# Performance work log

Measured on AMD Instinct MI355X. Metric: run time of the kernel, lower is better.

Reference implementation:

```python
import jax, jax.numpy as jnp
import numpy as np


def _mlp(x, W1, b1, W2, b2, W3, b3):
    # flatten -> fc(784,512) -> relu -> fc(512,128) -> relu -> fc(128,C)
    h = x.reshape(x.shape[0], -1)
    h = jax.nn.relu(h @ W1.T + b1)
    h = jax.nn.relu(h @ W2.T + b2)
    return h @ W3.T + b3


def setup_inputs() -> dict:
    key = jax.random.key(0)
    ks = jax.random.split(key, 6)
    B, Bu, C, D = 65536, 4096, 10, 28 * 28
    return {
        "x": jax.random.uniform(ks[0], (B, 28, 28), jnp.float32),
        "y": jax.random.randint(ks[1], (B,), 0, C),
        "x_unlab": jax.random.uniform(ks[2], (Bu, 28, 28), jnp.float32),
        "W1": jax.random.normal(ks[3], (512, D), jnp.float32) * 0.03,
        "b1": jnp.zeros((512,), jnp.float32),
        "W2": jax.random.normal(ks[4], (128, 512), jnp.float32) * 0.05,
        "b2": jnp.zeros((128,), jnp.float32),
        "W3": jax.random.normal(ks[5], (C, 128), jnp.float32) * 0.08,
        "b3": jnp.zeros((C,), jnp.float32),
    }


def reference(x, y, x_unlab, W1, b1, W2, b2, W3, b3):
    n_classes = W3.shape[0]
    # ---- labeled branch: BCEWithLogitsLoss(mean) vs one-hot targets ----
    logits = _mlp(x, W1, b1, W2, b2, W3, b3)  # [B, C]
    t = jax.nn.one_hot(y, n_classes, dtype=logits.dtype)
    bce = jnp.mean(jnp.maximum(logits, 0.0) - logits * t
                   + jnp.log1p(jnp.exp(-jnp.abs(logits))))
    # ---- unlabeled branch: semantic loss ----
    # sem_loss(probs): s[c] = sum_i p_i[c] * prod_{j != i} (1 - p_j[c]);
    # return mean over classes of -log(s). Done in log domain with a single
    # O(Bu) leave-one-out sum instead of the original O(Bu^2) double loop.
    o_u = _mlp(x_unlab, W1, b1, W2, b2, W3, b3)       # [Bu, C]
    logp = jax.nn.log_sigmoid(o_u)                     # log p
    log1mp = jax.nn.log_sigmoid(-o_u)                  # log (1 - p)
    loo = jnp.sum(log1mp, axis=0, keepdims=True) - log1mp  # leave-one-out log-prod
    log_s = jax.scipy.special.logsumexp(logp + loo, axis=0)  # [C]
    sl = jnp.mean(-log_s)
    # compute_loss returns (bce, sl); stacked here as a length-2 vector
    return jnp.stack([bce, sl])
```

## Files before the change

### kernel.cpp

```cpp
#include <hip/hip_runtime.h>
#include <hip/hip_bf16.h>
#include <stdint.h>

typedef unsigned short ushort_t;
typedef __bf16 bf16x8 __attribute__((ext_vector_type(8)));
typedef float f32x4 __attribute__((ext_vector_type(4)));

__device__ __forceinline__ ushort_t f2bf(float f) {
    union { float f; unsigned u; } v; v.f = f;
    unsigned u = v.u;
    unsigned r = u + 0x7fffu + ((u >> 16) & 1u);
    return (ushort_t)(r >> 16);
}
__device__ __forceinline__ float bf2f(ushort_t h) {
    union { unsigned u; float f; } v; v.u = ((unsigned)h) << 16;
    return v.f;
}
__device__ __forceinline__ unsigned packbf(float a, float b) {
    return ((unsigned)f2bf(b) << 16) | f2bf(a);
}

#define GLDS16(gsrc, ldst)                                                    \
    __builtin_amdgcn_global_load_lds(                                         \
        (const __attribute__((address_space(1))) void*)(gsrc),                \
        (__attribute__((address_space(3))) void*)(ldst), 16, 0, 0)

__global__ __launch_bounds__(256) void prep_kernel(
    const float* __restrict__ W1, const float* __restrict__ W2,
    ushort_t* __restrict__ W1p, ushort_t* __restrict__ W2b,
    float* __restrict__ stats)
{
    int idx = blockIdx.x * 256 + threadIdx.x;
    if (idx < 512 * 800) {
        int n = idx / 800, k = idx - n * 800;
        W1p[idx] = (k < 784) ? f2bf(W1[n * 784 + k]) : (ushort_t)0;
    }
    if (idx < 128 * 512) W2b[idx] = f2bf(W2[idx]);
    if (idx == 0) stats[0] = 0.0f;
}

#define AS_STRIDE 36
#define H_STRIDE  136

__global__ __launch_bounds__(256) void fused_kernel(
    const float* __restrict__ x, const float* __restrict__ xu,
    const ushort_t* __restrict__ W1p, const ushort_t* __restrict__ W2b,
    const float* __restrict__ b1, const float* __restrict__ b2,
    const int* __restrict__ y, const float* __restrict__ W3,
    const float* __restrict__ b3,
    float* __restrict__ stats, float* __restrict__ logits_u)
{
    __shared__ ushort_t smem[2 * 64 * AS_STRIDE + 2 * 128 * 32];
    __shared__ float W3s[1280];
    __shared__ float b3s[10];
    __shared__ float red[4];

    ushort_t* As0 = smem;
    ushort_t* As1 = smem + 64 * AS_STRIDE;
    ushort_t* Bs0 = smem + 2 * 64 * AS_STRIDE;
    ushort_t* Bs1 = Bs0 + 128 * 32;
    ushort_t* hs  = smem;

    const int tid = threadIdx.x;
    const int w = tid >> 6, lane = tid & 63;
    const int wm = w >> 1, wn = w & 1;
    const int quad = lane >> 4, lc = lane & 15;
    const int row_in = lane >> 2;
    const int koff = (lane & 3) * 8;
    const int tile = blockIdx.x;
    const size_t m0 = (size_t)tile * 64;

    for (int i = tid; i < 1280; i += 256) W3s[i] = W3[i];
    if (tid < 10) b3s[tid] = b3[tid];

    const int arow = tid >> 2;
    const int akoff = (tid & 3) * 8;
    const size_t grow = m0 + arow;
    const float* asrc = (grow < 65536) ? (x + grow * 784)
                                       : (xu + (grow - 65536) * 784);
    ushort_t* adst0 = &As0[arow * AS_STRIDE + akoff];
    ushort_t* adst1 = &As1[arow * AS_STRIDE + akoff];

    f32x4 h2acc[2][4];
#pragma unroll
    for (int i = 0; i < 2; i++)
#pragma unroll
        for (int j = 0; j < 4; j++)
#pragma unroll
            for (int r = 0; r < 4; r++) h2acc[i][j][r] = 0.0f;

    for (int nc = 0; nc < 4; nc++) {
        f32x4 acc[2][4];
#pragma unroll
        for (int i = 0; i < 2; i++)
#pragma unroll
            for (int j = 0; j < 4; j++)
#pragma unroll
                for (int r = 0; r < 4; r++) acc[i][j][r] = 0.0f;

        float4 p0a, p0b, p1a, p1b;
        {
            const float4* q0 = (const float4*)(asrc + akoff);
            p0a = q0[0]; p0b = q0[1];
            const float4* q1 = (const float4*)(asrc + 32 + akoff);
            p1a = q1[0]; p1b = q1[1];
        }

        for (int k0 = 0; k0 < 800; k0 += 64) {
            const bool has2 = (k0 + 32) < 800;
#pragma unroll
            for (int c = 0; c < 2; c++) {
                int row = (w * 2 + c) * 16 + row_in;
                const ushort_t* srcB =
                    W1p + (size_t)(nc * 128 + row) * 800 + k0 + koff;
                GLDS16(srcB, &Bs0[(w * 2 + c) * 512]);
            }
            if (has2) {
#pragma unroll
                for (int c = 0; c < 2; c++) {
                    int row = (w * 2 + c) * 16 + row_in;
                    const ushort_t* srcB =
                        W1p + (size_t)(nc * 128 + row) * 800 + k0 + 32 + koff;
                    GLDS16(srcB, &Bs1[(w * 2 + c) * 512]);
                }
            }
            {
                uint4 u;
                if (k0 + akoff <= 776) {
                    u.x = packbf(p0a.x, p0a.y);
                    u.y = packbf(p0a.z, p0a.w);
                    u.z = packbf(p0b.x, p0b.y);
                    u.w = packbf(p0b.z, p0b.w);
                } else {
                    u = make_uint4(0, 0, 0, 0);
                }
                *(uint4*)adst0 = u;
            }
            if (has2) {
                uint4 u;
                if (k0 + 32 + akoff <= 776) {
                    u.x = packbf(p1a.x, p1a.y);
                    u.y = packbf(p1a.z, p1a.w);
                    u.z = packbf(p1b.x, p1b.y);
                    u.w = packbf(p1b.z, p1b.w);
                } else {
                    u = make_uint4(0, 0, 0, 0);
                }
                *(uint4*)adst1 = u;
            }
            {
                int kn0 = k0 + 64 + akoff;
                if (kn0 <= 776) {
                    const float4* q = (const float4*)(asrc + kn0);
                    p0a = q[0]; p0b = q[1];
                }
                int kn1 = k0 + 96 + akoff;
                if (kn1 <= 776) {
                    const float4* q = (const float4*)(asrc + kn1);
                    p1a = q[0]; p1b = q[1];
                }
            }
            __syncthreads();
            {
                bf16x8 af[2], bfr[4];
#pragma unroll
                for (int i = 0; i < 2; i++)
                    af[i] = *(const bf16x8*)
                        &As0[(wm * 32 + i * 16 + lc) * AS_STRIDE + quad * 8];
#pragma unroll
                for (int j = 0; j < 4; j++)
                    bfr[j] = *(const bf16x8*)
                        &Bs0[(wn * 64 + j * 16 + lc) * 32 + quad * 8];
#pragma unroll
                for (int i = 0; i < 2; i++)
#pragma unroll
                    for (int j = 0; j < 4; j++)
                        acc[i][j] = __builtin_amdgcn_mfma_f32_16x16x32_bf16(
                            af[i], bfr[j], acc[i][j], 0, 0, 0);
            }
            if (has2) {
                bf16x8 af[2], bfr[4];
#pragma unroll
                for (int i = 0; i < 2; i++)
                    af[i] = *(const bf16x8*)
                        &As1[(wm * 32 + i * 16 + lc) * AS_STRIDE + quad * 8];
#pragma unroll
                for (int j = 0; j < 4; j++)
                    bfr[j] = *(const bf16x8*)
                        &Bs1[(wn * 64 + j * 16 + lc) * 32 + quad * 8];
#pragma unroll
                for (int i = 0; i < 2; i++)
#pragma unroll
                    for (int j = 0; j < 4; j++)
                        acc[i][j] = __builtin_amdgcn_mfma_f32_16x16x32_bf16(
                            af[i], bfr[j], acc[i][j], 0, 0, 0);
            }
            __syncthreads();
        }

        {
            float bias[4];
#pragma unroll
            for (int j = 0; j < 4; j++)
                bias[j] = b1[nc * 128 + wn * 64 + j * 16 + lc];
#pragma unroll
            for (int i = 0; i < 2; i++) {
                int r0 = wm * 32 + i * 16 + quad * 4;
#pragma unroll
                for (int j = 0; j < 4; j++) {
                    int col = wn * 64 + j * 16 + lc;
#pragma unroll
                    for (int r = 0; r < 4; r++) {
                        float v = fmaxf(acc[i][j][r] + bias[j], 0.0f);
                        hs[(r0 + r) * H_STRIDE + col] = f2bf(v);
                    }
                }
            }
        }
        __syncthreads();

#pragma unroll
        for (int p = 0; p < 4; p++) {
            bf16x8 af[2], bfr[4];
#pragma unroll
            for (int i = 0; i < 2; i++)
                af[i] = *(const bf16x8*)
                    &hs[(wm * 32 + i * 16 + lc) * H_STRIDE + p * 32 + quad * 8];
#pragma unroll
            for (int j = 0; j < 4; j++)
                bfr[j] = *(const bf16x8*)
                    (W2b + (size_t)(wn * 64 + j * 16 + lc) * 512
                         + nc * 128 + p * 32 + quad * 8);
#pragma unroll
            for (int i = 0; i < 2; i++)
#pragma unroll
                for (int j = 0; j < 4; j++)
                    h2acc[i][j] = __builtin_amdgcn_mfma_f32_16x16x32_bf16(
                        af[i], bfr[j], h2acc[i][j], 0, 0, 0);
        }
        __syncthreads();
    }

    {
        float bias[4];
#pragma unroll
        for (int j = 0; j < 4; j++) bias[j] = b2[wn * 64 + j * 16 + lc];
#pragma unroll
        for (int i = 0; i < 2; i++) {
            int r0 = wm * 32 + i * 16 + quad * 4;
#pragma unroll
            for (int j = 0; j < 4; j++) {
                int col = wn * 64 + j * 16 + lc;
#pragma unroll
                for (int r = 0; r < 4; r++) {
                    float v = fmaxf(h2acc[i][j][r] + bias[j], 0.0f);
                    hs[(r0 + r) * H_STRIDE + col] = f2bf(v);
                }
            }
        }
    }
    __syncthreads();

    float bce_part = 0.0f;
    for (int o = tid; o < 640; o += 256) {
        int r = o / 10, c = o - r * 10;
        size_t grw = m0 + r;
        float a = b3s[c];
        const ushort_t* hr = &hs[r * H_STRIDE];
        const float* wr = &W3s[c * 128];
#pragma unroll 8
        for (int k = 0; k < 128; k++) a += bf2f(hr[k]) * wr[k];
        if (grw < 65536) {
            float t = (y[grw] == c) ? 1.0f : 0.0f;
            bce_part += fmaxf(a, 0.0f) - a * t + log1pf(__expf(-fabsf(a)));
        } else {
            logits_u[(grw - 65536) * 10 + c] = a;
        }
    }
#pragma unroll
    for (int s = 32; s > 0; s >>= 1) bce_part += __shfl_down(bce_part, s, 64);
    if ((tid & 63) == 0) red[tid >> 6] = bce_part;
    __syncthreads();
    if (tid == 0) atomicAdd(stats, red[0] + red[1] + red[2] + red[3]);
}

__global__ __launch_bounds__(640) void finisher_kernel(
    const float* __restrict__ logits_u, const float* __restrict__ stats,
    float* __restrict__ out)
{
    __shared__ float Rs[64][10];
    __shared__ float Rm[64][10];
    __shared__ float Scol[10], Mcol[10];

    const int tid = threadIdx.x;
    const int g = tid / 10, c = tid - g * 10;
    float s = 0.0f, m = -1e30f;
    for (int i = g; i < 4096; i += 64) {
        float o = logits_u[i * 10 + c];
        s += fminf(-o, 0.0f) - log1pf(__expf(-fabsf(o)));
        m = fmaxf(m, o);
    }
    Rs[g][c] = s;
    Rm[g][c] = m;
    __syncthreads();
    if (tid < 10) {
        float ss = 0.0f, mm = -1e30f;
        for (int gg = 0; gg < 64; gg++) {
            ss += Rs[gg][tid];
            mm = fmaxf(mm, Rm[gg][tid]);
        }
        Scol[tid] = ss;
        Mcol[tid] = mm;
    }
    __syncthreads();
    float e = 0.0f;
    float mm = Mcol[c];
    for (int i = g; i < 4096; i += 64)
        e += __expf(logits_u[i * 10 + c] - mm);
    Rs[g][c] = e;
    __syncthreads();
    if (tid == 0) {
        float sl = 0.0f;
        for (int cc = 0; cc < 10; cc++) {
            float ee = 0.0f;
            for (int gg = 0; gg < 64; gg++) ee += Rs[gg][cc];
            sl += -(Scol[cc] + Mcol[cc] + __logf(ee));
        }
        sl *= 0.1f;
        out[0] = stats[0] * (1.0f / (65536.0f * 10.0f));
        out[1] = sl;
    }
}

extern "C" void kernel_launch(void* const* d_in, const int* in_sizes, int n_in,
                              void* d_out, int out_size, void* d_ws,
                              size_t ws_size, hipStream_t stream)
{
    const float* x  = (const float*)d_in[0];
    const int*   y  = (const int*)d_in[1];
    const float* xu = (const float*)d_in[2];
    const float* W1 = (const float*)d_in[3];
    const float* b1 = (const float*)d_in[4];
    const float* W2 = (const float*)d_in[5];
    const float* b2 = (const float*)d_in[6];
    const float* W3 = (const float*)d_in[7];
    const float* b3 = (const float*)d_in[8];
    float* out = (float*)d_out;

    char* ws = (char*)d_ws;
    ushort_t* W1p      = (ushort_t*)(ws + 0);
    ushort_t* W2b      = (ushort_t*)(ws + 819200);
    float*    stats    = (float*)(ws + 950272);
    float*    logits_u = (float*)(ws + 950528);

    prep_kernel<<<1600, 256, 0, stream>>>(W1, W2, W1p, W2b, stats);
    fused_kernel<<<1088, 256, 0, stream>>>(x, xu, W1p, W2b, b1, b2, y, W3, b3,
                                           stats, logits_u);
    finisher_kernel<<<1, 640, 0, stream>>>(logits_u, stats, out);
    (void)in_sizes; (void)n_in; (void)out_size; (void)ws_size;
}
```

Measured before the change: 576.3 us.

## Enlarge fused MLP row tile to 128 rows with 512-thread blocks

Each block now processes 128 input rows with 8 waves (2x4 warp grid) instead of 64 rows with 4 waves, halving the grid to 544 blocks. Every W1 tile streamed into shared memory is reused across twice as many rows, which cuts W1 and W2 reload traffic per row. In exchange there are fewer blocks to spread across the CUs, more shared memory per block and a per-wave shape of 4x2 fragments. Register pressure is now constrained by launch_bounds(512,2).

```diff
diff --git a/kernel.cpp b/kernel.cpp
--- a/kernel.cpp
+++ b/kernel.cpp
@@ -42,7 +42,7 @@
 #define AS_STRIDE 36
 #define H_STRIDE  136
 
-__global__ __launch_bounds__(256) void fused_kernel(
+__global__ __launch_bounds__(512, 2) void fused_kernel(
     const float* __restrict__ x, const float* __restrict__ xu,
     const ushort_t* __restrict__ W1p, const ushort_t* __restrict__ W2b,
     const float* __restrict__ b1, const float* __restrict__ b2,
@@ -50,27 +50,27 @@
     const float* __restrict__ b3,
     float* __restrict__ stats, float* __restrict__ logits_u)
 {
-    __shared__ ushort_t smem[2 * 64 * AS_STRIDE + 2 * 128 * 32];
+    __shared__ ushort_t smem[17408];
     __shared__ float W3s[1280];
     __shared__ float b3s[10];
-    __shared__ float red[4];
+    __shared__ float red[8];
 
     ushort_t* As0 = smem;
-    ushort_t* As1 = smem + 64 * AS_STRIDE;
-    ushort_t* Bs0 = smem + 2 * 64 * AS_STRIDE;
-    ushort_t* Bs1 = Bs0 + 128 * 32;
+    ushort_t* As1 = smem + 4608;
+    ushort_t* Bs0 = smem + 9216;
+    ushort_t* Bs1 = smem + 13312;
     ushort_t* hs  = smem;
 
     const int tid = threadIdx.x;
     const int w = tid >> 6, lane = tid & 63;
-    const int wm = w >> 1, wn = w & 1;
+    const int wm = w >> 2, wn = w & 3;
     const int quad = lane >> 4, lc = lane & 15;
     const int row_in = lane >> 2;
     const int koff = (lane & 3) * 8;
     const int tile = blockIdx.x;
-    const size_t m0 = (size_t)tile * 64;
-
-    for (int i = tid; i < 1280; i += 256) W3s[i] = W3[i];
+    const size_t m0 = (size_t)tile * 128;
+
+    for (int i = tid; i < 1280; i += 512) W3s[i] = W3[i];
     if (tid < 10) b3s[tid] = b3[tid];
 
     const int arow = tid >> 2;
@@ -81,20 +81,20 @@
     ushort_t* adst0 = &As0[arow * AS_STRIDE + akoff];
     ushort_t* adst1 = &As1[arow * AS_STRIDE + akoff];
 
-    f32x4 h2acc[2][4];
-#pragma unroll
-    for (int i = 0; i < 2; i++)
-#pragma unroll
-        for (int j = 0; j < 4; j++)
+    f32x4 h2acc[4][2];
+#pragma unroll
+    for (int i = 0; i < 4; i++)
+#pragma unroll
+        for (int j = 0; j < 2; j++)
 #pragma unroll
             for (int r = 0; r < 4; r++) h2acc[i][j][r] = 0.0f;
 
     for (int nc = 0; nc < 4; nc++) {
-        f32x4 acc[2][4];
-#pragma unroll
-        for (int i = 0; i < 2; i++)
-#pragma unroll
-            for (int j = 0; j < 4; j++)
+        f32x4 acc[4][2];
+#pragma unroll
+        for (int i = 0; i < 4; i++)
+#pragma unroll
+            for (int j = 0; j < 2; j++)
 #pragma unroll
                 for (int r = 0; r < 4; r++) acc[i][j][r] = 0.0f;
 
@@ -110,18 +110,14 @@
             const bool has2 = (k0 + 32) < 800;
 #pragma unroll
             for (int c = 0; c < 2; c++) {
-                int row = (w * 2 + c) * 16 + row_in;
-                const ushort_t* srcB =
-                    W1p + (size_t)(nc * 128 + row) * 800 + k0 + koff;
-                GLDS16(srcB, &Bs0[(w * 2 + c) * 512]);
-            }
-            if (has2) {
-#pragma unroll
-                for (int c = 0; c < 2; c++) {
-                    int row = (w * 2 + c) * 16 + row_in;
+                int q = w * 2 + c;
+                int p = q >> 3;
+                int rg = q & 7;
+                if (p == 0 || has2) {
+                    int row = rg * 16 + row_in;
                     const ushort_t* srcB =
-                        W1p + (size_t)(nc * 128 + row) * 800 + k0 + 32 + koff;
-                    GLDS16(srcB, &Bs1[(w * 2 + c) * 512]);
+                        W1p + (size_t)(nc * 128 + row) * 800 + k0 + p * 32 + koff;
+                    GLDS16(srcB, (p ? Bs1 : Bs0) + rg * 512);
                 }
             }
             {
@@ -162,36 +158,36 @@
             }
             __syncthreads();
             {
-                bf16x8 af[2], bfr[4];
-#pragma unroll
-                for (int i = 0; i < 2; i++)
+                bf16x8 af[4], bfr[2];
+#pragma unroll
+                for (int i = 0; i < 4; i++)
                     af[i] = *(const bf16x8*)
-                        &As0[(wm * 32 + i * 16 + lc) * AS_STRIDE + quad * 8];
-#pragma unroll
-                for (int j = 0; j < 4; j++)
+                        &As0[(wm * 64 + i * 16 + lc) * AS_STRIDE + quad * 8];
+#pragma unroll
+                for (int j = 0; j < 2; j++)
                     bfr[j] = *(const bf16x8*)
-                        &Bs0[(wn * 64 + j * 16 + lc) * 32 + quad * 8];
-#pragma unroll
-                for (int i = 0; i < 2; i++)
-#pragma unroll
-                    for (int j = 0; j < 4; j++)
+                        &Bs0[(wn * 32 + j * 16 + lc) * 32 + quad * 8];
+#pragma unroll
+                for (int i = 0; i < 4; i++)
+#pragma unroll
+                    for (int j = 0; j < 2; j++)
                         acc[i][j] = __builtin_amdgcn_mfma_f32_16x16x32_bf16(
                             af[i], bfr[j], acc[i][j], 0, 0, 0);
             }
             if (has2) {
-                bf16x8 af[2], bfr[4];
-#pragma unroll
-                for (int i = 0; i < 2; i++)
+                bf16x8 af[4], bfr[2];
+#pragma unroll
+                for (int i = 0; i < 4; i++)
                     af[i] = *(const bf16x8*)
-                        &As1[(wm * 32 + i * 16 + lc) * AS_STRIDE + quad * 8];
-#pragma unroll
-                for (int j = 0; j < 4; j++)
+                        &As1[(wm * 64 + i * 16 + lc) * AS_STRIDE + quad * 8];
+#pragma unroll
+                for (int j = 0; j < 2; j++)
                     bfr[j] = *(const bf16x8*)
-                        &Bs1[(wn * 64 + j * 16 + lc) * 32 + quad * 8];
-#pragma unroll
-                for (int i = 0; i < 2; i++)
-#pragma unroll
-                    for (int j = 0; j < 4; j++)
+                        &Bs1[(wn * 32 + j * 16 + lc) * 32 + quad * 8];
+#pragma unroll
+                for (int i = 0; i < 4; i++)
+#pragma unroll
+                    for (int j = 0; j < 2; j++)
                         acc[i][j] = __builtin_amdgcn_mfma_f32_16x16x32_bf16(
                             af[i], bfr[j], acc[i][j], 0, 0, 0);
             }
@@ -199,16 +195,16 @@
         }
 
         {
-            float bias[4];
-#pragma unroll
-            for (int j = 0; j < 4; j++)
-                bias[j] = b1[nc * 128 + wn * 64 + j * 16 + lc];
-#pragma unroll
-            for (int i = 0; i < 2; i++) {
-                int r0 = wm * 32 + i * 16 + quad * 4;
-#pragma unroll
-                for (int j = 0; j < 4; j++) {
-                    int col = wn * 64 + j * 16 + lc;
+            float bias[2];
+#pragma unroll
+            for (int j = 0; j < 2; j++)
+                bias[j] = b1[nc * 128 + wn * 32 + j * 16 + lc];
+#pragma unroll
+            for (int i = 0; i < 4; i++) {
+                int r0 = wm * 64 + i * 16 + quad * 4;
+#pragma unroll
+                for (int j = 0; j < 2; j++) {
+                    int col = wn * 32 + j * 16 + lc;
 #pragma unroll
                     for (int r = 0; r < 4; r++) {
                         float v = fmaxf(acc[i][j][r] + bias[j], 0.0f);
@@ -221,20 +217,20 @@
 
 #pragma unroll
         for (int p = 0; p < 4; p++) {
-            bf16x8 af[2], bfr[4];
-#pragma unroll
-            for (int i = 0; i < 2; i++)
+            bf16x8 af[4], bfr[2];
+#pragma unroll
+            for (int i = 0; i < 4; i++)
                 af[i] = *(const bf16x8*)
-                    &hs[(wm * 32 + i * 16 + lc) * H_STRIDE + p * 32 + quad * 8];
-#pragma unroll
-            for (int j = 0; j < 4; j++)
+                    &hs[(wm * 64 + i * 16 + lc) * H_STRIDE + p * 32 + quad * 8];
+#pragma unroll
+            for (int j = 0; j < 2; j++)
                 bfr[j] = *(const bf16x8*)
-                    (W2b + (size_t)(wn * 64 + j * 16 + lc) * 512
+                    (W2b + (size_t)(wn * 32 + j * 16 + lc) * 512
                          + nc * 128 + p * 32 + quad * 8);
 #pragma unroll
-            for (int i = 0; i < 2; i++)
-#pragma unroll
-                for (int j = 0; j < 4; j++)
+            for (int i = 0; i < 4; i++)
+#pragma unroll
+                for (int j = 0; j < 2; j++)
                     h2acc[i][j] = __builtin_amdgcn_mfma_f32_16x16x32_bf16(
                         af[i], bfr[j], h2acc[i][j], 0, 0, 0);
         }
@@ -242,15 +238,15 @@
     }
 
     {
-        float bias[4];
-#pragma unroll
-        for (int j = 0; j < 4; j++) bias[j] = b2[wn * 64 + j * 16 + lc];
-#pragma unroll
-        for (int i = 0; i < 2; i++) {
-            int r0 = wm * 32 + i * 16 + quad * 4;
-#pragma unroll
-            for (int j = 0; j < 4; j++) {
-                int col = wn * 64 + j * 16 + lc;
+        float bias[2];
+#pragma unroll
+        for (int j = 0; j < 2; j++) bias[j] = b2[wn * 32 + j * 16 + lc];
+#pragma unroll
+        for (int i = 0; i < 4; i++) {
+            int r0 = wm * 64 + i * 16 + quad * 4;
+#pragma unroll
+            for (int j = 0; j < 2; j++) {
+                int col = wn * 32 + j * 16 + lc;
 #pragma unroll
                 for (int r = 0; r < 4; r++) {
                     float v = fmaxf(h2acc[i][j][r] + bias[j], 0.0f);
@@ -262,7 +258,7 @@
     __syncthreads();
 
     float bce_part = 0.0f;
-    for (int o = tid; o < 640; o += 256) {
+    for (int o = tid; o < 1280; o += 512) {
         int r = o / 10, c = o - r * 10;
         size_t grw = m0 + r;
         float a = b3s[c];
@@ -281,7 +277,12 @@
     for (int s = 32; s > 0; s >>= 1) bce_part += __shfl_down(bce_part, s, 64);
     if ((tid & 63) == 0) red[tid >> 6] = bce_part;
     __syncthreads();
-    if (tid == 0) atomicAdd(stats, red[0] + red[1] + red[2] + red[3]);
+    if (tid == 0) {
+        float v = 0.0f;
+#pragma unroll
+        for (int i = 0; i < 8; i++) v += red[i];
+        atomicAdd(stats, v);
+    }
 }
 
 __global__ __launch_bounds__(640) void finisher_kernel(
@@ -354,8 +355,8 @@
     float*    logits_u = (float*)(ws + 950528);
 
     prep_kernel<<<1600, 256, 0, stream>>>(W1, W2, W1p, W2b, stats);
-    fused_kernel<<<1088, 256, 0, stream>>>(x, xu, W1p, W2b, b1, b2, y, W3, b3,
-                                           stats, logits_u);
+    fused_kernel<<<544, 512, 0, stream>>>(x, xu, W1p, W2b, b1, b2, y, W3, b3,
+                                          stats, logits_u);
     finisher_kernel<<<1, 640, 0, stream>>>(logits_u, stats, out);
     (void)in_sizes; (void)n_in; (void)out_size; (void)ws_size;
 }
```

New measurement: 812.7 us. 1.41x slower.
